# Optimization experiments

Measured on AMD Instinct MI355X. Metric: run time of the kernel, lower is better.

Reference implementation:

```python
import jax, jax.numpy as jnp
import numpy as np

WIRE_DIM = 32
NUM_WIRES = 64
BATCH = 8192


def setup_inputs() -> dict:
    key = jax.random.key(0)
    k1, k2, k3, k4 = jax.random.split(key, 4)
    outputs = jax.random.normal(k1, (BATCH, NUM_WIRES * WIRE_DIM), dtype=jnp.float32)
    tests = jax.random.randint(k2, (BATCH, 2), 0, NUM_WIRES, dtype=jnp.int64)
    W1 = jax.random.normal(k3, (2 * WIRE_DIM, 10), dtype=jnp.float32) * 0.1
    b1 = jnp.zeros((10,), dtype=jnp.float32)
    W2 = jax.random.normal(k4, (10, 1), dtype=jnp.float32) * 0.1
    b2 = jnp.zeros((1,), dtype=jnp.float32)
    return {"outputs": outputs, "tests": tests, "W1": W1, "b1": b1, "W2": W2, "b2": b2}


def reference(outputs, tests, W1, b1, W2, b2):
    B = outputs.shape[0]
    W = outputs.shape[1] // WIRE_DIM          # num_wires
    wires = outputs.reshape(B, W, WIRE_DIM)   # [B, W, D]
    person = tests[:, 0]
    location = tests[:, 1]
    # gather_nd equivalent: person wire vector per batch element
    person_vec = wires[jnp.arange(B), person]                 # [B, D]
    # per-wire concat [person_vec, wire_vec] -> shared tiny MLP, vectorized over wires
    x = jnp.concatenate(
        [jnp.broadcast_to(person_vec[:, None, :], (B, W, WIRE_DIM)), wires], axis=-1
    )                                                          # [B, W, 2D]
    h = jax.nn.relu(jnp.einsum("bwd,dh->bwh", x, W1) + b1)     # [B, W, 10]
    logits = (jnp.einsum("bwh,ho->bwo", h, W2) + b2)[..., 0]   # [B, W]
    # sparse softmax cross entropy with location labels
    loss = -jnp.take_along_axis(jax.nn.log_softmax(logits, axis=-1),
                                location[:, None], axis=-1)[:, 0]  # [B]
    return loss
```

## Files before the change

kernel.cpp:

```cpp
#include <hip/hip_runtime.h>

#define WIRE_DIM  32
#define NUM_WIRES 64
#define BATCH     8192
#define HID       10
#define STRIDE    36
#define NWAVES    4096

__device__ __forceinline__ float rl(float x, int slane) {
    return __uint_as_float(__builtin_amdgcn_readlane(__float_as_uint(x), slane));
}

__global__ __launch_bounds__(256) void isnet_kernel(
    const float* __restrict__ outputs,
    const int*   __restrict__ tests,
    const float* __restrict__ W1,
    const float* __restrict__ bias1,
    const float* __restrict__ W2,
    const float* __restrict__ bias2,
    float*       __restrict__ out)
{
    __shared__ __align__(16) float stage[4][NUM_WIRES * STRIDE];

    const int tid  = threadIdx.x;
    const int lane = tid & 63;
    const int wave = tid >> 6;
    float* buf = stage[wave];

    const int w0 = blockIdx.x * 4 + wave;
    const int r  = lane >> 3;
    const int cc = lane & 7;

    auto run = [&](int bb) {
        const int sp = __builtin_amdgcn_readfirstlane(tests[2 * bb]);
        const int sl = __builtin_amdgcn_readfirstlane(tests[2 * bb + 1]);

        float acc[HID];
        #pragma unroll
        for (int h = 0; h < HID; ++h) acc[h] = bias1[h];

        #pragma unroll 1
        for (int j = 0; j < 8; ++j) {
            float4 x = *(const float4*)&buf[lane * STRIDE + j * 4];
            float4 p = *(const float4*)&buf[sp   * STRIDE + j * 4];
            const float* wp = W1 + (4 * j) * HID;
            const float* ww = W1 + (32 + 4 * j) * HID;
            #pragma unroll
            for (int h = 0; h < HID; ++h) {
                acc[h] += p.x * wp[0 * HID + h] + p.y * wp[1 * HID + h]
                        + p.z * wp[2 * HID + h] + p.w * wp[3 * HID + h]
                        + x.x * ww[0 * HID + h] + x.y * ww[1 * HID + h]
                        + x.z * ww[2 * HID + h] + x.w * ww[3 * HID + h];
            }
        }

        float v = bias2[0];
        #pragma unroll
        for (int h = 0; h < HID; ++h) v += fmaxf(acc[h], 0.f) * W2[h];

        float m = v;
        #pragma unroll
        for (int off = 32; off > 0; off >>= 1) m = fmaxf(m, __shfl_xor(m, off));
        float s = __expf(v - m);
        #pragma unroll
        for (int off = 32; off > 0; off >>= 1) s += __shfl_xor(s, off);
        float lv = rl(v, sl);
        if (lane == 0) out[bb] = m + __logf(s) - lv;
    };

    float4 c[8];

    const float* g1 = outputs + (size_t)w0 * (NUM_WIRES * WIRE_DIM) + lane * 4;
    #pragma unroll
    for (int t = 0; t < 8; ++t) c[t] = *(const float4*)(g1 + t * 256);
    #pragma unroll
    for (int t = 0; t < 8; ++t)
        *(float4*)&buf[(t * 8 + r) * STRIDE + cc * 4] = c[t];

    const float* g2 = outputs + (size_t)(w0 + NWAVES) * (NUM_WIRES * WIRE_DIM)
                    + lane * 4;
    #pragma unroll
    for (int t = 0; t < 8; ++t) c[t] = *(const float4*)(g2 + t * 256);

    run(w0);

    #pragma unroll
    for (int t = 0; t < 8; ++t)
        *(float4*)&buf[(t * 8 + r) * STRIDE + cc * 4] = c[t];

    run(w0 + NWAVES);
}

extern "C" void kernel_launch(void* const* d_in, const int* in_sizes, int n_in,
                              void* d_out, int out_size, void* d_ws, size_t ws_size,
                              hipStream_t stream) {
    const float* outputs = (const float*)d_in[0];
    const int*   tests   = (const int*)d_in[1];
    const float* W1      = (const float*)d_in[2];
    const float* b1      = (const float*)d_in[3];
    const float* W2      = (const float*)d_in[4];
    const float* b2      = (const float*)d_in[5];
    float* out = (float*)d_out;

    isnet_kernel<<<NWAVES / 4, 256, 0, stream>>>(
        outputs, tests, W1, b1, W2, b2, out);
}
```

Baseline: 102.7 us.

## Use one batch row per wave and fully unroll the MLP reduction

Replaces the two-rows-per-wave software-pipelined scheme, where the second row's global loads overlapped the first row's compute, with one row per wave across twice as many blocks. It also loads all eight x and p float4 vectors from LDS up front and fully unrolls the j loop. The aim is more waves in flight to hide memory latency through occupancy rather than manual prefetch. The cost is more registers per thread from the unrolled loop, which may lower occupancy, and the loss of explicit load/compute overlap within a wave.

```diff
diff --git a/kernel.cpp b/kernel.cpp
--- a/kernel.cpp
+++ b/kernel.cpp
@@ -5,7 +5,6 @@
 #define BATCH     8192
 #define HID       10
 #define STRIDE    36
-#define NWAVES    4096
 
 __device__ __forceinline__ float rl(float x, int slane) {
     return __uint_as_float(__builtin_amdgcn_readlane(__float_as_uint(x), slane));
@@ -27,68 +26,60 @@
     const int wave = tid >> 6;
     float* buf = stage[wave];
 
-    const int w0 = blockIdx.x * 4 + wave;
+    const int b = blockIdx.x * 4 + wave;
+
+    const int sp = __builtin_amdgcn_readfirstlane(tests[2 * b]);
+    const int sl = __builtin_amdgcn_readfirstlane(tests[2 * b + 1]);
+
+    const float* g = outputs + (size_t)b * (NUM_WIRES * WIRE_DIM) + lane * 4;
     const int r  = lane >> 3;
     const int cc = lane & 7;
+    {
+        float4 c[8];
+        #pragma unroll
+        for (int t = 0; t < 8; ++t) c[t] = *(const float4*)(g + t * 256);
+        #pragma unroll
+        for (int t = 0; t < 8; ++t)
+            *(float4*)&buf[(t * 8 + r) * STRIDE + cc * 4] = c[t];
+    }
 
-    auto run = [&](int bb) {
-        const int sp = __builtin_amdgcn_readfirstlane(tests[2 * bb]);
-        const int sl = __builtin_amdgcn_readfirstlane(tests[2 * bb + 1]);
-
-        float acc[HID];
-        #pragma unroll
-        for (int h = 0; h < HID; ++h) acc[h] = bias1[h];
-
-        #pragma unroll 1
-        for (int j = 0; j < 8; ++j) {
-            float4 x = *(const float4*)&buf[lane * STRIDE + j * 4];
-            float4 p = *(const float4*)&buf[sp   * STRIDE + j * 4];
-            const float* wp = W1 + (4 * j) * HID;
-            const float* ww = W1 + (32 + 4 * j) * HID;
-            #pragma unroll
-            for (int h = 0; h < HID; ++h) {
-                acc[h] += p.x * wp[0 * HID + h] + p.y * wp[1 * HID + h]
-                        + p.z * wp[2 * HID + h] + p.w * wp[3 * HID + h]
-                        + x.x * ww[0 * HID + h] + x.y * ww[1 * HID + h]
-                        + x.z * ww[2 * HID + h] + x.w * ww[3 * HID + h];
-            }
-        }
-
-        float v = bias2[0];
-        #pragma unroll
-        for (int h = 0; h < HID; ++h) v += fmaxf(acc[h], 0.f) * W2[h];
-
-        float m = v;
-        #pragma unroll
-        for (int off = 32; off > 0; off >>= 1) m = fmaxf(m, __shfl_xor(m, off));
-        float s = __expf(v - m);
-        #pragma unroll
-        for (int off = 32; off > 0; off >>= 1) s += __shfl_xor(s, off);
-        float lv = rl(v, sl);
-        if (lane == 0) out[bb] = m + __logf(s) - lv;
-    };
-
-    float4 c[8];
-
-    const float* g1 = outputs + (size_t)w0 * (NUM_WIRES * WIRE_DIM) + lane * 4;
-    #pragma unroll
-    for (int t = 0; t < 8; ++t) c[t] = *(const float4*)(g1 + t * 256);
+    float4 x[8], p[8];
     #pragma unroll
     for (int t = 0; t < 8; ++t)
-        *(float4*)&buf[(t * 8 + r) * STRIDE + cc * 4] = c[t];
+        x[t] = *(const float4*)&buf[lane * STRIDE + t * 4];
+    #pragma unroll
+    for (int t = 0; t < 8; ++t)
+        p[t] = *(const float4*)&buf[sp * STRIDE + t * 4];
 
-    const float* g2 = outputs + (size_t)(w0 + NWAVES) * (NUM_WIRES * WIRE_DIM)
-                    + lane * 4;
+    float acc[HID];
     #pragma unroll
-    for (int t = 0; t < 8; ++t) c[t] = *(const float4*)(g2 + t * 256);
-
-    run(w0);
+    for (int h = 0; h < HID; ++h) acc[h] = bias1[h];
 
     #pragma unroll
-    for (int t = 0; t < 8; ++t)
-        *(float4*)&buf[(t * 8 + r) * STRIDE + cc * 4] = c[t];
+    for (int j = 0; j < 8; ++j) {
+        const float* wp = W1 + (4 * j) * HID;
+        const float* ww = W1 + (32 + 4 * j) * HID;
+        #pragma unroll
+        for (int h = 0; h < HID; ++h) {
+            acc[h] += p[j].x * wp[0 * HID + h] + p[j].y * wp[1 * HID + h]
+                    + p[j].z * wp[2 * HID + h] + p[j].w * wp[3 * HID + h]
+                    + x[j].x * ww[0 * HID + h] + x[j].y * ww[1 * HID + h]
+                    + x[j].z * ww[2 * HID + h] + x[j].w * ww[3 * HID + h];
+        }
+    }
 
-    run(w0 + NWAVES);
+    float v = bias2[0];
+    #pragma unroll
+    for (int h = 0; h < HID; ++h) v += fmaxf(acc[h], 0.f) * W2[h];
+
+    float m = v;
+    #pragma unroll
+    for (int off = 32; off > 0; off >>= 1) m = fmaxf(m, __shfl_xor(m, off));
+    float s = __expf(v - m);
+    #pragma unroll
+    for (int off = 32; off > 0; off >>= 1) s += __shfl_xor(s, off);
+    float lv = rl(v, sl);
+    if (lane == 0) out[b] = m + __logf(s) - lv;
 }
 
 extern "C" void kernel_launch(void* const* d_in, const int* in_sizes, int n_in,
@@ -102,6 +93,6 @@
     const float* b2      = (const float*)d_in[5];
     float* out = (float*)d_out;
 
-    isnet_kernel<<<NWAVES / 4, 256, 0, stream>>>(
+    isnet_kernel<<<BATCH / 4, 256, 0, stream>>>(
         outputs, tests, W1, b1, W2, b2, out);
 }
```

Result: no change. 103.9 us (+1.2%).
